# Kernel tuning notes

Hardware: AMD Instinct MI355X
Metric: run time of the kernel (lower is better)

## Reference

```python
import jax, jax.numpy as jnp
import numpy as np

HEADS, DIM_HEAD = 8, 96
DIM = HEADS * DIM_HEAD            # 768
DEPTH = 8
MEM_LAYERS = (4, 5)               # layers with KNN-retrieval attention
TOPK = 32                         # num_retrieved_memories
CLIP_LEN, PREFIX_LEN = 10, 10
NEG = -1e9


def layernorm(x, g, b):
    m = x.mean(-1, keepdims=True)
    v = ((x - m) ** 2).mean(-1, keepdims=True)
    return (x - m) * jax.lax.rsqrt(v + 1e-5) * g + b


def attention(x, wq_l, wkv_l, wo_l, mem_k=None, mem_v=None):
    # one-headed key/values (memorizing-transformers style), multi-head queries
    b, n, _ = x.shape
    q = (x @ wq_l).reshape(b, n, HEADS, DIM_HEAD).transpose(0, 2, 1, 3)  # [b,h,n,d]
    q = q * (DIM_HEAD ** -0.5)
    kv = x @ wkv_l                                   # [b,n,2d]
    k, v = kv[..., :DIM_HEAD], kv[..., DIM_HEAD:]    # [b,n,d] each
    sim = jnp.einsum('bhid,bjd->bhij', q, k)         # local scores
    causal = jnp.tril(jnp.ones((n, n), dtype=bool))
    sim = jnp.where(causal, sim, NEG)
    if mem_k is not None:
        # exact inner-product top-k retrieval from per-batch memory bank
        mem_sim = jnp.einsum('bhid,bmd->bhim', q, mem_k)      # [b,h,n,M]
        top_sim, top_idx = jax.lax.top_k(mem_sim, TOPK)       # [b,h,n,K]
        mem_v_sel = jnp.take_along_axis(
            mem_v[:, None, None], top_idx[..., None], axis=3)  # [b,h,n,K,d]
        attn = jax.nn.softmax(jnp.concatenate([top_sim, sim], axis=-1), axis=-1)
        mem_attn, loc_attn = attn[..., :TOPK], attn[..., TOPK:]
        out = (jnp.einsum('bhij,bhijd->bhid', mem_attn, mem_v_sel)
               + jnp.einsum('bhij,bjd->bhid', loc_attn, v))
    else:
        attn = jax.nn.softmax(sim, axis=-1)
        out = jnp.einsum('bhij,bjd->bhid', attn, v)
    out = out.transpose(0, 2, 1, 3).reshape(b, n, DIM)
    return out @ wo_l


def setup_inputs() -> dict:
    key = jax.random.key(0)
    ks = jax.random.split(key, 12)
    s = 0.02
    inp = {
        'x': jax.random.normal(ks[0], (16, 640), jnp.float32),
        'linear_w': jax.random.normal(ks[1], (640, CLIP_LEN * DIM), jnp.float32) * s,
        'linear_b': jnp.zeros((CLIP_LEN * DIM,), jnp.float32),
        'prefix_const': jax.random.normal(ks[2], (PREFIX_LEN, DIM), jnp.float32),
        'ln1_g': jnp.ones((DEPTH, DIM), jnp.float32),
        'ln1_b': jnp.zeros((DEPTH, DIM), jnp.float32),
        'wq': jax.random.normal(ks[3], (DEPTH, DIM, DIM), jnp.float32) * s,
        'wkv': jax.random.normal(ks[4], (DEPTH, DIM, 2 * DIM_HEAD), jnp.float32) * s,
        'wo': jax.random.normal(ks[5], (DEPTH, DIM, DIM), jnp.float32) * s,
        'ln2_g': jnp.ones((DEPTH, DIM), jnp.float32),
        'ln2_b': jnp.zeros((DEPTH, DIM), jnp.float32),
        'w1': jax.random.normal(ks[6], (DEPTH, DIM, 4 * DIM), jnp.float32) * s,
        'b1': jnp.zeros((DEPTH, 4 * DIM), jnp.float32),
        'w2': jax.random.normal(ks[7], (DEPTH, 4 * DIM, DIM), jnp.float32) * s,
        'b2': jnp.zeros((DEPTH, DIM), jnp.float32),
        'lnf_g': jnp.ones((DIM,), jnp.float32),
        'lnf_b': jnp.zeros((DIM,), jnp.float32),
        'mem_k': jax.random.normal(ks[8], (16, 32768, DIM_HEAD), jnp.float32),
        'mem_v': jax.random.normal(ks[9], (16, 32768, DIM_HEAD), jnp.float32),
    }
    return inp


def reference(x, linear_w, linear_b, prefix_const,
              ln1_g, ln1_b, wq, wkv, wo, ln2_g, ln2_b,
              w1, b1, w2, b2, lnf_g, lnf_b, mem_k, mem_v):
    b = x.shape[0]
    # linear projection of clip feature -> clip_length tokens
    h = (x @ linear_w + linear_b).reshape(b, CLIP_LEN, DIM)
    prefix = jnp.broadcast_to(prefix_const[None], (b, PREFIX_LEN, DIM))
    t = jnp.concatenate([h, prefix], axis=1)  # [b, 20, dim]
    for l in range(DEPTH):
        mk, mv = (mem_k, mem_v) if l in MEM_LAYERS else (None, None)
        t = t + attention(layernorm(t, ln1_g[l], ln1_b[l]), wq[l], wkv[l], wo[l], mk, mv)
        hf = layernorm(t, ln2_g[l], ln2_b[l])
        t = t + (jax.nn.gelu(hf @ w1[l] + b1[l]) @ w2[l] + b2[l])
    t = layernorm(t, lnf_g, lnf_b)
    return t[:, CLIP_LEN:]  # [b, prefix_length, dim]
```

## Files before the change

kernel.cpp:

```cpp
#include <hip/hip_runtime.h>
#include <hip/hip_bf16.h>

#define BB 16
#define NSEQ 20
#define HEADS 8
#define DH 96
#define DIM 768
#define FF 3072
#define KMEM 32768
#define NCHUNK 4
#define CHUNK 8192
#define CAP 128

typedef __attribute__((ext_vector_type(8))) short short8v;
typedef __attribute__((ext_vector_type(4))) float f32x4;

__device__ __forceinline__ short f2b(float x) {
    __hip_bfloat16 h = __float2bfloat16(x);
    return *reinterpret_cast<short*>(&h);
}

__global__ __launch_bounds__(256) void gemm_mfma(const float* __restrict__ A, const float* __restrict__ B,
    const float* __restrict__ bias, const float* __restrict__ resid, float* __restrict__ C,
    int M, int N, int K, int lda, int ldc, float scale, int act)
{
    int tid = threadIdx.x;
    int w = tid >> 6, lane = tid & 63;
    int m0 = blockIdx.y * 16;
    int n0 = blockIdx.x * 128 + w * 32;
    int row = lane & 15;
    int kg  = lane >> 4;
    const float* arow = A + (size_t)(m0 + row) * lda;
    int c0 = n0 + row;
    int c1 = n0 + 16 + row;
    int c0c = min(c0, N - 1);
    int c1c = min(c1, N - 1);
    f32x4 acc0 = {0.f, 0.f, 0.f, 0.f};
    f32x4 acc1 = {0.f, 0.f, 0.f, 0.f};

    for (int k0 = 0; k0 < K; k0 += 32) {
        int kb = k0 + kg * 8;
        float av[8];
        *(float4*)(av)     = *(const float4*)(arow + kb);
        *(float4*)(av + 4) = *(const float4*)(arow + kb + 4);
        const float* bp0 = B + c0c;
        const float* bp1 = B + c1c;
        float bv0[8], bv1[8];
#pragma unroll
        for (int j = 0; j < 8; j++) {
            bv0[j] = bp0[(size_t)(kb + j) * N];
            bv1[j] = bp1[(size_t)(kb + j) * N];
        }
        short8v af, b0f, b1f;
#pragma unroll
        for (int j = 0; j < 8; j++) {
            af[j]  = f2b(av[j]);
            b0f[j] = f2b(bv0[j]);
            b1f[j] = f2b(bv1[j]);
        }
        acc0 = __builtin_amdgcn_mfma_f32_16x16x32_bf16(af, b0f, acc0, 0, 0, 0);
        acc1 = __builtin_amdgcn_mfma_f32_16x16x32_bf16(af, b1f, acc1, 0, 0, 0);
    }

#pragma unroll
    for (int r = 0; r < 4; r++) {
        int rw = m0 + kg * 4 + r;
        if (c0 < N) {
            float v = acc0[r] * scale;
            if (bias) v += bias[c0];
            if (act) {
                float xx = v;
                float tt = 0.7978845608028654f * (xx + 0.044715f * xx * xx * xx);
                v = 0.5f * xx * (1.0f + tanhf(tt));
            }
            if (resid) v += resid[(size_t)rw * ldc + c0];
            C[(size_t)rw * ldc + c0] = v;
        }
        if (c1 < N) {
            float v = acc1[r] * scale;
            if (bias) v += bias[c1];
            if (act) {
                float xx = v;
                float tt = 0.7978845608028654f * (xx + 0.044715f * xx * xx * xx);
                v = 0.5f * xx * (1.0f + tanhf(tt));
            }
            if (resid) v += resid[(size_t)rw * ldc + c1];
            C[(size_t)rw * ldc + c1] = v;
        }
    }
}

__global__ __launch_bounds__(256) void ln_k(const float* __restrict__ x, const float* __restrict__ g,
    const float* __restrict__ bb, float* __restrict__ y)
{
    int row = blockIdx.x;
    const float* xr = x + (size_t)row * DIM;
    int tid = threadIdx.x;
    float v0 = xr[tid], v1 = xr[tid + 256], v2 = xr[tid + 512];
    __shared__ float red[4];
    float s = v0 + v1 + v2;
    for (int off = 32; off; off >>= 1) s += __shfl_down(s, off);
    if ((tid & 63) == 0) red[tid >> 6] = s;
    __syncthreads();
    float mean = (red[0] + red[1] + red[2] + red[3]) * (1.f / 768.f);
    __syncthreads();
    float d0 = v0 - mean, d1 = v1 - mean, d2 = v2 - mean;
    s = d0 * d0 + d1 * d1 + d2 * d2;
    for (int off = 32; off; off >>= 1) s += __shfl_down(s, off);
    if ((tid & 63) == 0) red[tid >> 6] = s;
    __syncthreads();
    float var = (red[0] + red[1] + red[2] + red[3]) * (1.f / 768.f);
    float rs = rsqrtf(var + 1e-5f);
    float* yr = y + (size_t)row * DIM;
    yr[tid]       = d0 * rs * g[tid]       + bb[tid];
    yr[tid + 256] = d1 * rs * g[tid + 256] + bb[tid + 256];
    yr[tid + 512] = d2 * rs * g[tid + 512] + bb[tid + 512];
}

__global__ __launch_bounds__(256) void lnf_k(const float* __restrict__ x, const float* __restrict__ g,
    const float* __restrict__ bb, float* __restrict__ out)
{
    int blk = blockIdx.x;
    int b = blk / 10, ii = blk - b * 10;
    int row = b * NSEQ + 10 + ii;
    const float* xr = x + (size_t)row * DIM;
    int tid = threadIdx.x;
    float v0 = xr[tid], v1 = xr[tid + 256], v2 = xr[tid + 512];
    __shared__ float red[4];
    float s = v0 + v1 + v2;
    for (int off = 32; off; off >>= 1) s += __shfl_down(s, off);
    if ((tid & 63) == 0) red[tid >> 6] = s;
    __syncthreads();
    float mean = (red[0] + red[1] + red[2] + red[3]) * (1.f / 768.f);
    __syncthreads();
    float d0 = v0 - mean, d1 = v1 - mean, d2 = v2 - mean;
    s = d0 * d0 + d1 * d1 + d2 * d2;
    for (int off = 32; off; off >>= 1) s += __shfl_down(s, off);
    if ((tid & 63) == 0) red[tid >> 6] = s;
    __syncthreads();
    float var = (red[0] + red[1] + red[2] + red[3]) * (1.f / 768.f);
    float rs = rsqrtf(var + 1e-5f);
    float* orow = out + ((size_t)(b * 10 + ii)) * DIM;
    orow[tid]       = d0 * rs * g[tid]       + bb[tid];
    orow[tid + 256] = d1 * rs * g[tid + 256] + bb[tid + 256];
    orow[tid + 512] = d2 * rs * g[tid + 512] + bb[tid + 512];
}

__global__ __launch_bounds__(256) void prefix_k(const float* __restrict__ p, float* __restrict__ t)
{
    int idx = blockIdx.x * 256 + threadIdx.x;
    if (idx < BB * 7680) {
        int b = idx / 7680;
        int r = idx - b * 7680;
        t[(size_t)b * (NSEQ * DIM) + 7680 + r] = p[r];
    }
}

__global__ __launch_bounds__(256) void lattn_k(const float* __restrict__ q, const float* __restrict__ kv,
    float* __restrict__ ao)
{
    int b = blockIdx.x, h = blockIdx.y;
    __shared__ float sims[NSEQ][NSEQ];
    __shared__ float probs[NSEQ][NSEQ];
    const float* qb = q + (size_t)b * NSEQ * DIM + h * DH;
    const float* kb = kv + (size_t)b * NSEQ * 192;
    int tid = threadIdx.x;
    for (int p = tid; p < NSEQ * NSEQ; p += 256) {
        int i = p / NSEQ, j = p - i * NSEQ;
        float s;
        if (j > i) s = -1.0e9f;
        else {
            s = 0.f;
            for (int d = 0; d < DH; d++) s = fmaf(qb[(size_t)i * DIM + d], kb[j * 192 + d], s);
        }
        sims[i][j] = s;
    }
    __syncthreads();
    if (tid < NSEQ) {
        int i = tid;
        float m = -1e30f;
        for (int j = 0; j < NSEQ; j++) m = fmaxf(m, sims[i][j]);
        float sum = 0.f;
        for (int j = 0; j < NSEQ; j++) { float e = expf(sims[i][j] - m); probs[i][j] = e; sum += e; }
        float inv = 1.f / sum;
        for (int j = 0; j < NSEQ; j++) probs[i][j] *= inv;
    }
    __syncthreads();
    for (int p = tid; p < NSEQ * DH; p += 256) {
        int i = p / DH, d = p - i * DH;
        float o = 0.f;
        for (int j = 0; j <= i; j++) o = fmaf(probs[i][j], kb[j * 192 + 96 + d], o);
        ao[((size_t)b * NSEQ + i) * DIM + h * DH + d] = o;
    }
}

__device__ __forceinline__ bool tk_better(float va, int ia, float vb, int ib) {
    return (va > vb) || (va == vb && ia < ib);
}

__device__ __forceinline__ void lds_fence() {
    asm volatile("s_waitcnt lgkmcnt(0)" ::: "memory");
    __builtin_amdgcn_sched_barrier(0);
}

__device__ void topk32(float* bv, int* bi, int cnt, int lane,
                       float& ov, int& oi, float& thr_out) {
    lds_fence();
    float v0 = (lane < cnt)      ? bv[lane]      : -3.0e38f;
    int   i0 = (lane < cnt)      ? bi[lane]      : 0x7fffffff;
    float v1 = (lane + 64 < cnt) ? bv[lane + 64] : -3.0e38f;
    int   i1 = (lane + 64 < cnt) ? bi[lane + 64] : 0x7fffffff;
    lds_fence();
#pragma unroll
    for (int k = 2; k <= 128; k <<= 1) {
#pragma unroll
        for (int j = 64; j >= 1; j >>= 1) {
            if (j >= k) continue;
            if (j == 64) {
                bool asc = ((lane & k) == 0);
                bool b01 = tk_better(v0, i0, v1, i1);
                if (b01 != asc) { float tv = v0; int ti = i0; v0 = v1; i0 = i1; v1 = tv; i1 = ti; }
            } else {
                {
                    float pv = __shfl_xor(v0, j); int pi = __shfl_xor(i0, j);
                    bool asc = ((lane & k) == 0);
                    bool first = ((lane & j) == 0);
                    bool mb = tk_better(v0, i0, pv, pi);
                    bool keep = first ? (mb == asc) : (mb != asc);
                    if (!keep) { v0 = pv; i0 = pi; }
                }
                {
                    float pv = __shfl_xor(v1, j); int pi = __shfl_xor(i1, j);
                    bool asc = (((lane + 64) & k) == 0);
                    bool first = ((lane & j) == 0);
                    bool mb = tk_better(v1, i1, pv, pi);
                    bool keep = first ? (mb == asc) : (mb != asc);
                    if (!keep) { v1 = pv; i1 = pi; }
                }
            }
        }
    }
    if (lane < 32) { bv[lane] = v0; bi[lane] = i0; }
    lds_fence();
    ov = v0; oi = i0;
    thr_out = __shfl(v0, 31);
}

__device__ __forceinline__ void tk_pass(const float4 kr[6], const float4 qreg[5][6],
    float thrR[5], int cntR[5], float (*bufv)[CAP], int (*bufi)[CAP],
    int r0, int lane, int qt, int key)
{
    float a[5];
#pragma unroll
    for (int rr = 0; rr < 5; rr++) a[rr] = 0.f;
#pragma unroll
    for (int i = 0; i < 6; i++) {
        float4 kv = kr[i];
#pragma unroll
        for (int rr = 0; rr < 5; rr++) {
            float4 qv = qreg[rr][i];
            a[rr] = fmaf(qv.x, kv.x, a[rr]);
            a[rr] = fmaf(qv.y, kv.y, a[rr]);
            a[rr] = fmaf(qv.z, kv.z, a[rr]);
            a[rr] = fmaf(qv.w, kv.w, a[rr]);
        }
    }
#pragma unroll
    for (int rr = 0; rr < 5; rr++) {
        a[rr] += __shfl_xor(a[rr], 1);
        a[rr] += __shfl_xor(a[rr], 2);
    }
#pragma unroll
    for (int rr = 0; rr < 5; rr++) {
        bool cand = (qt == 0) && (a[rr] >= thrR[rr]);
        unsigned long long mask = __ballot(cand);
        int n = __popcll(mask);
        if (n) {
            int r = r0 + rr;
            if (cntR[rr] + n > CAP) {
                float dv; int di;
                topk32(&bufv[r][0], &bufi[r][0], cntR[rr], lane, dv, di, thrR[rr]);
                cntR[rr] = 32;
            }
            int pos = cntR[rr] + __popcll(mask & ((1ull << lane) - 1ull));
            if (cand) { bufv[r][pos] = a[rr]; bufi[r][pos] = key; }
            cntR[rr] += n;
        }
    }
}

__global__ __launch_bounds__(256, 2) void memtopk_k(const float* __restrict__ q, const float* __restrict__ memk,
    float* __restrict__ tkv, int* __restrict__ tki)
{
    __shared__ float bufv[NSEQ][CAP];
    __shared__ int   bufi[NSEQ][CAP];
    int c = blockIdx.x, h = blockIdx.y, b = blockIdx.z;
    int tid = threadIdx.x;
    int lane = tid & 63;
    int w = tid >> 6;
    int r0 = w * 5;
    int qt = lane & 3;
    int kk = lane >> 2;

    float4 qreg[5][6];
#pragma unroll
    for (int rr = 0; rr < 5; rr++) {
        const float4* qrow = (const float4*)(q + ((size_t)(b * NSEQ + r0 + rr)) * DIM + h * DH + qt * 24);
#pragma unroll
        for (int i = 0; i < 6; i++) qreg[rr][i] = qrow[i];
    }

    float thrR[5]; int cntR[5];
#pragma unroll
    for (int rr = 0; rr < 5; rr++) { thrR[rr] = -3.0e38f; cntR[rr] = 0; }

    const float* kbase = memk + (size_t)b * KMEM * DH;
    int k0 = c * CHUNK;

    float4 ka[6], kb2[6];
    {
        const float4* kp = (const float4*)(kbase + (size_t)(k0 + kk) * DH + qt * 24);
#pragma unroll
        for (int i = 0; i < 6; i++) ka[i] = kp[i];
    }
    for (int p = 0; p < CHUNK / 16; p += 2) {
        int key0 = k0 + p * 16 + kk;
        {
            const float4* kp = (const float4*)(kbase + (size_t)(key0 + 16) * DH + qt * 24);
#pragma unroll
            for (int i = 0; i < 6; i++) kb2[i] = kp[i];
        }
        tk_pass(ka, qreg, thrR, cntR, bufv, bufi, r0, lane, qt, key0);
        if (p + 2 < CHUNK / 16) {
            const float4* kp = (const float4*)(kbase + (size_t)(key0 + 32) * DH + qt * 24);
#pragma unroll
            for (int i = 0; i < 6; i++) ka[i] = kp[i];
        }
        tk_pass(kb2, qreg, thrR, cntR, bufv, bufi, r0, lane, qt, key0 + 16);
    }
#pragma unroll
    for (int rr = 0; rr < 5; rr++) {
        int r = r0 + rr;
        float ov; int oi; float dthr;
        topk32(&bufv[r][0], &bufi[r][0], cntR[rr], lane, ov, oi, dthr);
        if (lane < 32) {
            size_t base = ((((size_t)b * HEADS + h) * NSEQ + r) * NCHUNK + c) * 32;
            tkv[base + lane] = ov;
            tki[base + lane] = oi;
        }
    }
}

__global__ __launch_bounds__(64) void memattn_k(const float* __restrict__ q, const float* __restrict__ kv,
    const float* __restrict__ memv, const float* __restrict__ tkv, const int* __restrict__ tki,
    float* __restrict__ ao)
{
    int i = blockIdx.x, h = blockIdx.y, b = blockIdx.z;
    __shared__ float cv[NCHUNK * 32];
    __shared__ int   ci[NCHUNK * 32];
    __shared__ float selv[32];
    __shared__ int   seli[32];
    __shared__ float ls[NSEQ];
    __shared__ float probs[52];
    int tid = threadIdx.x;
    size_t base = (((size_t)b * HEADS + h) * NSEQ + i) * (NCHUNK * 32);
#pragma unroll
    for (int s = 0; s < NCHUNK * 32 / 64; s++) {
        cv[tid + 64 * s] = tkv[base + tid + 64 * s];
        ci[tid + 64 * s] = tki[base + tid + 64 * s];
    }
    const float* qr = q + ((size_t)b * NSEQ + i) * DIM + h * DH;
    const float* kvb = kv + (size_t)b * NSEQ * 192;
    if (tid <= i) {
        float s = 0.f;
        for (int d = 0; d < DH; d++) s = fmaf(qr[d], kvb[tid * 192 + d], s);
        ls[tid] = s;
    }
    __syncthreads();
    for (int r = 0; r < 32; r++) {
        float bv = -3.0e38f; int bidx = 0x7fffffff; int bs = 0;
#pragma unroll
        for (int s = 0; s < NCHUNK * 32 / 64; s++) {
            float v = cv[tid + 64 * s]; int ix = ci[tid + 64 * s];
            if (tk_better(v, ix, bv, bidx)) { bv = v; bidx = ix; bs = tid + 64 * s; }
        }
        for (int off = 32; off; off >>= 1) {
            float ovv = __shfl_down(bv, off);
            int oii = __shfl_down(bidx, off);
            int oss = __shfl_down(bs, off);
            if (tk_better(ovv, oii, bv, bidx)) { bv = ovv; bidx = oii; bs = oss; }
        }
        if (tid == 0) { selv[r] = bv; seli[r] = bidx; cv[bs] = -3.0e38f; }
        __syncthreads();
    }
    if (tid == 0) {
        float m = -1e30f;
        for (int r = 0; r < 32; r++) m = fmaxf(m, selv[r]);
        for (int j = 0; j <= i; j++) m = fmaxf(m, ls[j]);
        float sum = 0.f;
        for (int r = 0; r < 32; r++) { float e = expf(selv[r] - m); probs[r] = e; sum += e; }
        for (int j = 0; j <= i; j++) { float e = expf(ls[j] - m); probs[32 + j] = e; sum += e; }
        float inv = 1.f / sum;
        for (int r = 0; r < 32 + i + 1; r++) probs[r] *= inv;
    }
    __syncthreads();
    const float* mvb = memv + (size_t)b * KMEM * DH;
    for (int d = tid; d < DH; d += 64) {
        float o = 0.f;
        for (int r = 0; r < 32; r++) o = fmaf(probs[r], mvb[(size_t)seli[r] * DH + d], o);
        for (int j = 0; j <= i; j++) o = fmaf(probs[32 + j], kvb[j * 192 + 96 + d], o);
        ao[((size_t)b * NSEQ + i) * DIM + h * DH + d] = o;
    }
}

extern "C" void kernel_launch(void* const* d_in, const int* in_sizes, int n_in,
                              void* d_out, int out_size, void* d_ws, size_t ws_size,
                              hipStream_t stream) {
    const float* x            = (const float*)d_in[0];
    const float* linear_w     = (const float*)d_in[1];
    const float* linear_b     = (const float*)d_in[2];
    const float* prefix_const = (const float*)d_in[3];
    const float* ln1_g        = (const float*)d_in[4];
    const float* ln1_b        = (const float*)d_in[5];
    const float* wq           = (const float*)d_in[6];
    const float* wkv          = (const float*)d_in[7];
    const float* wo           = (const float*)d_in[8];
    const float* ln2_g        = (const float*)d_in[9];
    const float* ln2_b        = (const float*)d_in[10];
    const float* w1           = (const float*)d_in[11];
    const float* b1           = (const float*)d_in[12];
    const float* w2           = (const float*)d_in[13];
    const float* b2           = (const float*)d_in[14];
    const float* lnf_g        = (const float*)d_in[15];
    const float* lnf_b        = (const float*)d_in[16];
    const float* mem_k        = (const float*)d_in[17];
    const float* mem_v        = (const float*)d_in[18];

    float* ws = (float*)d_ws;
    float* t   = ws;
    float* y   = ws + 245760;
    float* qb  = ws + 491520;
    float* kvb = ws + 737280;
    float* ao  = ws + 798720;
    float* h1  = ws + 1044480;
    float* tkv = ws + 2027520;
    int*   tki = (int*)(ws + 2355200);
    float* out = (float*)d_out;

    const float qscale = 0.10206207261596577f;

    gemm_mfma<<<dim3(60, 1), 256, 0, stream>>>(x, linear_w, linear_b, nullptr, t,
                                               16, 7680, 640, 640, 15360, 1.f, 0);
    prefix_k<<<dim3(480), 256, 0, stream>>>(prefix_const, t);

    for (int l = 0; l < 8; l++) {
        ln_k<<<320, 256, 0, stream>>>(t, ln1_g + (size_t)l * DIM, ln1_b + (size_t)l * DIM, y);
        gemm_mfma<<<dim3(6, 20), 256, 0, stream>>>(y, wq + (size_t)l * DIM * DIM, nullptr, nullptr, qb,
                                                   320, 768, 768, 768, 768, qscale, 0);
        gemm_mfma<<<dim3(2, 20), 256, 0, stream>>>(y, wkv + (size_t)l * DIM * 192, nullptr, nullptr, kvb,
                                                   320, 192, 768, 768, 192, 1.f, 0);
        if (l == 4 || l == 5) {
            memtopk_k<<<dim3(NCHUNK, HEADS, BB), 256, 0, stream>>>(qb, mem_k, tkv, tki);
            memattn_k<<<dim3(NSEQ, HEADS, BB), 64, 0, stream>>>(qb, kvb, mem_v, tkv, tki, ao);
        } else {
            lattn_k<<<dim3(BB, HEADS), 256, 0, stream>>>(qb, kvb, ao);
        }
        gemm_mfma<<<dim3(6, 20), 256, 0, stream>>>(ao, wo + (size_t)l * DIM * DIM, nullptr, t, t,
                                                   320, 768, 768, 768, 768, 1.f, 0);
        ln_k<<<320, 256, 0, stream>>>(t, ln2_g + (size_t)l * DIM, ln2_b + (size_t)l * DIM, y);
        gemm_mfma<<<dim3(24, 20), 256, 0, stream>>>(y, w1 + (size_t)l * DIM * FF, b1 + (size_t)l * FF, nullptr, h1,
                                                    320, 3072, 768, 768, 3072, 1.f, 1);
        gemm_mfma<<<dim3(6, 20), 256, 0, stream>>>(h1, w2 + (size_t)l * FF * DIM, b2 + (size_t)l * DIM, t, t,
                                                   320, 768, 3072, 3072, 768, 1.f, 0);
    }
    lnf_k<<<160, 256, 0, stream>>>(t, lnf_g, lnf_b, out);
}
```

Before: 2.457 ms.

## Pre-transpose weights to bf16 and store activations in bf16 for MFMA GEMMs

Each layer's weights are converted each call into a transposed bf16 layout, so the GEMM loads contiguous 16-byte K-vectors instead of strided fp32 column reads with conversion in the inner loop. LayerNorm, attention outputs and the FFN hidden layer are written as bf16, which halves activation traffic. The memory top-k chunking also goes from 4 to 8 chunks. In exchange, extra conversion kernels run every call and re-read all weights once, and the workspace layout grows.

```diff
diff --git a/kernel.cpp b/kernel.cpp
--- a/kernel.cpp
+++ b/kernel.cpp
@@ -8,20 +8,65 @@
 #define DIM 768
 #define FF 3072
 #define KMEM 32768
-#define NCHUNK 4
-#define CHUNK 8192
+#define NCHUNK 8
+#define CHUNK 4096
 #define CAP 128
 
+typedef unsigned short u16;
 typedef __attribute__((ext_vector_type(8))) short short8v;
 typedef __attribute__((ext_vector_type(4))) float f32x4;
 
-__device__ __forceinline__ short f2b(float x) {
+__device__ __forceinline__ u16 f2bu(float x) {
     __hip_bfloat16 h = __float2bfloat16(x);
-    return *reinterpret_cast<short*>(&h);
-}
-
-__global__ __launch_bounds__(256) void gemm_mfma(const float* __restrict__ A, const float* __restrict__ B,
-    const float* __restrict__ bias, const float* __restrict__ resid, float* __restrict__ C,
+    return *reinterpret_cast<u16*>(&h);
+}
+
+__global__ __launch_bounds__(256) void conv_k(const float* __restrict__ src, u16* __restrict__ dst, int n)
+{
+    int i = blockIdx.x * 256 + threadIdx.x;
+    if (i < n) dst[i] = f2bu(src[i]);
+}
+
+__device__ __forceinline__ void tconv_tile(const float* __restrict__ src, u16* __restrict__ dst,
+                                           int K, int N, int kt, int nt, int tx, int ty)
+{
+    __shared__ float tile[32][33];
+    int k0 = kt * 32, n0 = nt * 32;
+#pragma unroll
+    for (int i = 0; i < 4; i++)
+        tile[ty + 8 * i][tx] = src[(size_t)(k0 + ty + 8 * i) * N + n0 + tx];
+    __syncthreads();
+#pragma unroll
+    for (int i = 0; i < 4; i++)
+        dst[(size_t)(n0 + ty + 8 * i) * K + k0 + tx] = f2bu(tile[tx][ty + 8 * i]);
+}
+
+__global__ __launch_bounds__(256) void tconv_k(const float* __restrict__ src, u16* __restrict__ dst, int K, int N)
+{
+    int tilesN = N >> 5;
+    tconv_tile(src, dst, K, N, blockIdx.x / tilesN, blockIdx.x % tilesN,
+               threadIdx.x & 31, threadIdx.x >> 5);
+}
+
+__global__ __launch_bounds__(256) void wconv5_k(const float* __restrict__ wq, const float* __restrict__ wkv,
+    const float* __restrict__ wo, const float* __restrict__ w1, const float* __restrict__ w2,
+    u16* __restrict__ wt)
+{
+    int bx = blockIdx.x;
+    int tx = threadIdx.x & 31, ty = threadIdx.x >> 5;
+    if (bx < 576)       tconv_tile(wq,  wt + 0,       768, 768,  bx / 24,          bx % 24,          tx, ty);
+    else if (bx < 720)  tconv_tile(wkv, wt + 589824,  768, 192,  (bx - 576) / 6,   (bx - 576) % 6,   tx, ty);
+    else if (bx < 1296) tconv_tile(wo,  wt + 737280,  768, 768,  (bx - 720) / 24,  (bx - 720) % 24,  tx, ty);
+    else if (bx < 3600) tconv_tile(w1,  wt + 1327104, 768, 3072, (bx - 1296) / 96, (bx - 1296) % 96, tx, ty);
+    else                tconv_tile(w2,  wt + 3686400, 3072, 768, (bx - 3600) / 24, (bx - 3600) % 24, tx, ty);
+}
+
+__device__ __forceinline__ void storeC(float* C, size_t idx, float v) { C[idx] = v; }
+__device__ __forceinline__ void storeC(u16* C, size_t idx, float v)   { C[idx] = f2bu(v); }
+
+template <typename CT>
+__global__ __launch_bounds__(256) void gemm_bt(const u16* __restrict__ A, const u16* __restrict__ Bt,
+    const float* __restrict__ bias, const float* __restrict__ resid, CT* __restrict__ C,
     int M, int N, int K, int lda, int ldc, float scale, int act)
 {
     int tid = threadIdx.x;
@@ -30,38 +75,21 @@
     int n0 = blockIdx.x * 128 + w * 32;
     int row = lane & 15;
     int kg  = lane >> 4;
-    const float* arow = A + (size_t)(m0 + row) * lda;
+    const u16* arow = A + (size_t)(m0 + row) * lda + kg * 8;
     int c0 = n0 + row;
     int c1 = n0 + 16 + row;
-    int c0c = min(c0, N - 1);
-    int c1c = min(c1, N - 1);
+    const u16* bt0 = Bt + (size_t)min(c0, N - 1) * K + kg * 8;
+    const u16* bt1 = Bt + (size_t)min(c1, N - 1) * K + kg * 8;
     f32x4 acc0 = {0.f, 0.f, 0.f, 0.f};
     f32x4 acc1 = {0.f, 0.f, 0.f, 0.f};
-
+#pragma unroll 2
     for (int k0 = 0; k0 < K; k0 += 32) {
-        int kb = k0 + kg * 8;
-        float av[8];
-        *(float4*)(av)     = *(const float4*)(arow + kb);
-        *(float4*)(av + 4) = *(const float4*)(arow + kb + 4);
-        const float* bp0 = B + c0c;
-        const float* bp1 = B + c1c;
-        float bv0[8], bv1[8];
-#pragma unroll
-        for (int j = 0; j < 8; j++) {
-            bv0[j] = bp0[(size_t)(kb + j) * N];
-            bv1[j] = bp1[(size_t)(kb + j) * N];
-        }
-        short8v af, b0f, b1f;
-#pragma unroll
-        for (int j = 0; j < 8; j++) {
-            af[j]  = f2b(av[j]);
-            b0f[j] = f2b(bv0[j]);
-            b1f[j] = f2b(bv1[j]);
-        }
-        acc0 = __builtin_amdgcn_mfma_f32_16x16x32_bf16(af, b0f, acc0, 0, 0, 0);
-        acc1 = __builtin_amdgcn_mfma_f32_16x16x32_bf16(af, b1f, acc1, 0, 0, 0);
-    }
-
+        short8v af = *(const short8v*)(arow + k0);
+        short8v b0 = *(const short8v*)(bt0 + k0);
+        short8v b1 = *(const short8v*)(bt1 + k0);
+        acc0 = __builtin_amdgcn_mfma_f32_16x16x32_bf16(af, b0, acc0, 0, 0, 0);
+        acc1 = __builtin_amdgcn_mfma_f32_16x16x32_bf16(af, b1, acc1, 0, 0, 0);
+    }
 #pragma unroll
     for (int r = 0; r < 4; r++) {
         int rw = m0 + kg * 4 + r;
@@ -74,7 +102,7 @@
                 v = 0.5f * xx * (1.0f + tanhf(tt));
             }
             if (resid) v += resid[(size_t)rw * ldc + c0];
-            C[(size_t)rw * ldc + c0] = v;
+            storeC(C, (size_t)rw * ldc + c0, v);
         }
         if (c1 < N) {
             float v = acc1[r] * scale;
@@ -85,13 +113,13 @@
                 v = 0.5f * xx * (1.0f + tanhf(tt));
             }
             if (resid) v += resid[(size_t)rw * ldc + c1];
-            C[(size_t)rw * ldc + c1] = v;
+            storeC(C, (size_t)rw * ldc + c1, v);
         }
     }
 }
 
 __global__ __launch_bounds__(256) void ln_k(const float* __restrict__ x, const float* __restrict__ g,
-    const float* __restrict__ bb, float* __restrict__ y)
+    const float* __restrict__ bb, u16* __restrict__ y)
 {
     int row = blockIdx.x;
     const float* xr = x + (size_t)row * DIM;
@@ -111,10 +139,10 @@
     __syncthreads();
     float var = (red[0] + red[1] + red[2] + red[3]) * (1.f / 768.f);
     float rs = rsqrtf(var + 1e-5f);
-    float* yr = y + (size_t)row * DIM;
-    yr[tid]       = d0 * rs * g[tid]       + bb[tid];
-    yr[tid + 256] = d1 * rs * g[tid + 256] + bb[tid + 256];
-    yr[tid + 512] = d2 * rs * g[tid + 512] + bb[tid + 512];
+    u16* yr = y + (size_t)row * DIM;
+    yr[tid]       = f2bu(d0 * rs * g[tid]       + bb[tid]);
+    yr[tid + 256] = f2bu(d1 * rs * g[tid + 256] + bb[tid + 256]);
+    yr[tid + 512] = f2bu(d2 * rs * g[tid + 512] + bb[tid + 512]);
 }
 
 __global__ __launch_bounds__(256) void lnf_k(const float* __restrict__ x, const float* __restrict__ g,
@@ -157,7 +185,7 @@
 }
 
 __global__ __launch_bounds__(256) void lattn_k(const float* __restrict__ q, const float* __restrict__ kv,
-    float* __restrict__ ao)
+    u16* __restrict__ ao)
 {
     int b = blockIdx.x, h = blockIdx.y;
     __shared__ float sims[NSEQ][NSEQ];
@@ -190,7 +218,7 @@
         int i = p / DH, d = p - i * DH;
         float o = 0.f;
         for (int j = 0; j <= i; j++) o = fmaf(probs[i][j], kb[j * 192 + 96 + d], o);
-        ao[((size_t)b * NSEQ + i) * DIM + h * DH + d] = o;
+        ao[((size_t)b * NSEQ + i) * DIM + h * DH + d] = f2bu(o);
     }
 }
 
@@ -353,7 +381,7 @@
 
 __global__ __launch_bounds__(64) void memattn_k(const float* __restrict__ q, const float* __restrict__ kv,
     const float* __restrict__ memv, const float* __restrict__ tkv, const int* __restrict__ tki,
-    float* __restrict__ ao)
+    u16* __restrict__ ao)
 {
     int i = blockIdx.x, h = blockIdx.y, b = blockIdx.z;
     __shared__ float cv[NCHUNK * 32];
@@ -409,7 +437,7 @@
         float o = 0.f;
         for (int r = 0; r < 32; r++) o = fmaf(probs[r], mvb[(size_t)seli[r] * DH + d], o);
         for (int j = 0; j <= i; j++) o = fmaf(probs[32 + j], kvb[j * 192 + 96 + d], o);
-        ao[((size_t)b * NSEQ + i) * DIM + h * DH + d] = o;
+        ao[((size_t)b * NSEQ + i) * DIM + h * DH + d] = f2bu(o);
     }
 }
 
@@ -437,41 +465,49 @@
     const float* mem_v        = (const float*)d_in[18];
 
     float* ws = (float*)d_ws;
-    float* t   = ws;
-    float* y   = ws + 245760;
-    float* qb  = ws + 491520;
-    float* kvb = ws + 737280;
-    float* ao  = ws + 798720;
-    float* h1  = ws + 1044480;
-    float* tkv = ws + 2027520;
-    int*   tki = (int*)(ws + 2355200);
-    float* out = (float*)d_out;
+    float* t    = ws;
+    u16*   yb   = (u16*)(ws + 245760);
+    float* qb   = ws + 491520;
+    float* kvb  = ws + 737280;
+    u16*   aob  = (u16*)(ws + 798720);
+    u16*   h1b  = (u16*)(ws + 1044480);
+    float* tkv  = ws + 2027520;
+    int*   tki  = (int*)(ws + 2682880);
+    u16*   wt   = (u16*)(ws + 3338240);
+    u16*   xb   = (u16*)(ws + 6361088);
+    float* out  = (float*)d_out;
 
     const float qscale = 0.10206207261596577f;
-
-    gemm_mfma<<<dim3(60, 1), 256, 0, stream>>>(x, linear_w, linear_b, nullptr, t,
-                                               16, 7680, 640, 640, 15360, 1.f, 0);
+    const size_t WQT = 0, WKVT = 589824, WOT = 737280, W1T = 1327104, W2T = 3686400;
+
+    conv_k<<<40, 256, 0, stream>>>(x, xb, 16 * 640);
+    tconv_k<<<4800, 256, 0, stream>>>(linear_w, wt, 640, 7680);
+    gemm_bt<float><<<dim3(60, 1), 256, 0, stream>>>(xb, wt, linear_b, nullptr, t,
+                                                    16, 7680, 640, 640, 15360, 1.f, 0);
     prefix_k<<<dim3(480), 256, 0, stream>>>(prefix_const, t);
 
     for (int l = 0; l < 8; l++) {
-        ln_k<<<320, 256, 0, stream>>>(t, ln1_g + (size_t)l * DIM, ln1_b + (size_t)l * DIM, y);
-        gemm_mfma<<<dim3(6, 20), 256, 0, stream>>>(y, wq + (size_t)l * DIM * DIM, nullptr, nullptr, qb,
-                                                   320, 768, 768, 768, 768, qscale, 0);
-        gemm_mfma<<<dim3(2, 20), 256, 0, stream>>>(y, wkv + (size_t)l * DIM * 192, nullptr, nullptr, kvb,
-                                                   320, 192, 768, 768, 192, 1.f, 0);
+        wconv5_k<<<5904, 256, 0, stream>>>(wq + (size_t)l * DIM * DIM, wkv + (size_t)l * DIM * 192,
+                                           wo + (size_t)l * DIM * DIM, w1 + (size_t)l * DIM * FF,
+                                           w2 + (size_t)l * FF * DIM, wt);
+        ln_k<<<320, 256, 0, stream>>>(t, ln1_g + (size_t)l * DIM, ln1_b + (size_t)l * DIM, yb);
+        gemm_bt<float><<<dim3(6, 20), 256, 0, stream>>>(yb, wt + WQT, nullptr, nullptr, qb,
+                                                        320, 768, 768, 768, 768, qscale, 0);
+        gemm_bt<float><<<dim3(2, 20), 256, 0, stream>>>(yb, wt + WKVT, nullptr, nullptr, kvb,
+                                                        320, 192, 768, 768, 192, 1.f, 0);
         if (l == 4 || l == 5) {
             memtopk_k<<<dim3(NCHUNK, HEADS, BB), 256, 0, stream>>>(qb, mem_k, tkv, tki);
-            memattn_k<<<dim3(NSEQ, HEADS, BB), 64, 0, stream>>>(qb, kvb, mem_v, tkv, tki, ao);
+            memattn_k<<<dim3(NSEQ, HEADS, BB), 64, 0, stream>>>(qb, kvb, mem_v, tkv, tki, aob);
         } else {
-            lattn_k<<<dim3(BB, HEADS), 256, 0, stream>>>(qb, kvb, ao);
-        }
-        gemm_mfma<<<dim3(6, 20), 256, 0, stream>>>(ao, wo + (size_t)l * DIM * DIM, nullptr, t, t,
-                                                   320, 768, 768, 768, 768, 1.f, 0);
-        ln_k<<<320, 256, 0, stream>>>(t, ln2_g + (size_t)l * DIM, ln2_b + (size_t)l * DIM, y);
-        gemm_mfma<<<dim3(24, 20), 256, 0, stream>>>(y, w1 + (size_t)l * DIM * FF, b1 + (size_t)l * FF, nullptr, h1,
-                                                    320, 3072, 768, 768, 3072, 1.f, 1);
-        gemm_mfma<<<dim3(6, 20), 256, 0, stream>>>(h1, w2 + (size_t)l * FF * DIM, b2 + (size_t)l * DIM, t, t,
-                                                   320, 768, 3072, 3072, 768, 1.f, 0);
+            lattn_k<<<dim3(BB, HEADS), 256, 0, stream>>>(qb, kvb, aob);
+        }
+        gemm_bt<float><<<dim3(6, 20), 256, 0, stream>>>(aob, wt + WOT, nullptr, t, t,
+                                                        320, 768, 768, 768, 768, 1.f, 0);
+        ln_k<<<320, 256, 0, stream>>>(t, ln2_g + (size_t)l * DIM, ln2_b + (size_t)l * DIM, yb);
+        gemm_bt<u16><<<dim3(24, 20), 256, 0, stream>>>(yb, wt + W1T, b1 + (size_t)l * FF, nullptr, h1b,
+                                                       320, 3072, 768, 768, 3072, 1.f, 1);
+        gemm_bt<float><<<dim3(6, 20), 256, 0, stream>>>(h1b, wt + W2T, b2 + (size_t)l * DIM, t, t,
+                                                        320, 768, 3072, 3072, 768, 1.f, 0);
     }
     lnf_k<<<160, 256, 0, stream>>>(t, lnf_g, lnf_b, out);
 }
```

New measurement: 2.298 ms. -6.5%, faster.
